# Kernel tuning notes

Measured on AMD Instinct MI355X. Metric: run time of the kernel, lower is better.

Reference implementation:

```python
import jax, jax.numpy as jnp
import numpy as np

N_NODES = 200000
N_EDGES = 400000
IN_CH, HID_CH, OUT_CH = 768, 256, 256
NUM_GRAPHS = 8000


def setup_inputs() -> dict:
    key = jax.random.key(0)
    k = jax.random.split(key, 8)
    x = jax.random.normal(k[0], (N_NODES, IN_CH), dtype=jnp.float32)
    edge_index = jax.random.randint(k[1], (2, N_EDGES), 0, N_NODES, dtype=jnp.int64)
    batch = jnp.sort(jax.random.randint(k[2], (N_NODES,), 0, NUM_GRAPHS, dtype=jnp.int64))
    # GCNConv params (Glorot-ish scale)
    W1 = jax.random.normal(k[3], (IN_CH, HID_CH), dtype=jnp.float32) / np.sqrt(IN_CH)
    b1 = jnp.zeros((HID_CH,), dtype=jnp.float32)
    W2 = jax.random.normal(k[4], (HID_CH, OUT_CH), dtype=jnp.float32) / np.sqrt(HID_CH)
    b2 = jnp.zeros((OUT_CH,), dtype=jnp.float32)
    return {"x": x, "W1": W1, "b1": b1, "W2": W2, "b2": b2,
            "edge_index": edge_index, "batch": batch}


def gcn_conv(x, W, b, src, dst, norm):
    # PyG GCNConv: linear transform, then normalized gather-scatter aggregation
    h = x @ W  # [N, C_out]
    msg = h[src] * norm[:, None]  # gather + scale, [E_sl, C_out]
    out = jax.ops.segment_sum(msg, dst, num_segments=N_NODES)  # scatter-add
    return out + b


def reference(x, W1, b1, W2, b2, edge_index, batch):
    # Add self-loops (PyG GCNConv default add_self_loops=True)
    loops = jnp.arange(N_NODES, dtype=edge_index.dtype)
    src = jnp.concatenate([edge_index[0], loops])
    dst = jnp.concatenate([edge_index[1], loops])
    # Symmetric degree normalization: deg computed on dst (incl. self-loops)
    deg = jax.ops.segment_sum(jnp.ones_like(dst, dtype=x.dtype), dst, num_segments=N_NODES)
    dinv = jnp.where(deg > 0, jax.lax.rsqrt(deg), 0.0)
    norm = dinv[src] * dinv[dst]  # [E_sl]

    h = gcn_conv(x, W1, b1, src, dst, norm)
    h = jax.nn.relu(h)
    h = gcn_conv(h, W2, b2, src, dst, norm)

    # global_mean_pool over batch vector
    sums = jax.ops.segment_sum(h, batch, num_segments=NUM_GRAPHS)
    counts = jax.ops.segment_sum(jnp.ones((N_NODES,), dtype=h.dtype), batch, num_segments=NUM_GRAPHS)
    return sums / jnp.maximum(counts, 1.0)[:, None]
```

## Files before the change

kernel.cpp:

```cpp
#include <hip/hip_runtime.h>


#define N_NODES_C 200000
#define N_EDGES_C 400000
#define IN_CH_C 768
#define HID_C 256
#define NUM_GRAPHS_C 8000

typedef __attribute__((ext_vector_type(8))) short short8;
typedef __attribute__((ext_vector_type(4))) float f32x4;

__device__ __forceinline__ unsigned short f2bf(float f) {
  union { float f; unsigned u; } v; v.f = f;
  unsigned r = v.u + 0x7FFFu + ((v.u >> 16) & 1u);
  return (unsigned short)(r >> 16);
}


__global__ void zero2_kernel(int* __restrict__ a, int* __restrict__ b, int n) {
  int i = blockIdx.x * blockDim.x + threadIdx.x;
  if (i < n) { a[i] = 0; b[i] = 0; }
}

__global__ void hist_kernel(const int* __restrict__ dst, int* __restrict__ deg, int E) {
  int e = blockIdx.x * blockDim.x + threadIdx.x;
  if (e < E) atomicAdd(&deg[dst[e]], 1);
}

__global__ void dinv_kernel(const int* __restrict__ deg, float* __restrict__ dinv, int n) {
  int i = blockIdx.x * blockDim.x + threadIdx.x;
  if (i < n) dinv[i] = rsqrtf((float)(deg[i] + 1));
}

__global__ __launch_bounds__(256) void scan1_kernel(const int* __restrict__ deg,
                                                    int* __restrict__ offs,
                                                    int* __restrict__ bsums, int n) {
  __shared__ int s[256];
  int tid = threadIdx.x;
  int i = blockIdx.x * 256 + tid;
  int v = (i < n) ? deg[i] : 0;
  s[tid] = v;
  __syncthreads();
  for (int d = 1; d < 256; d <<= 1) {
    int t = (tid >= d) ? s[tid - d] : 0;
    __syncthreads();
    s[tid] += t;
    __syncthreads();
  }
  if (i < n) offs[i] = s[tid] - v;
  if (tid == 255) bsums[blockIdx.x] = s[255];
}

__global__ __launch_bounds__(1024) void scan2_kernel(int* __restrict__ bsums, int nb) {
  __shared__ int s[1024];
  int tid = threadIdx.x;
  int v = (tid < nb) ? bsums[tid] : 0;
  s[tid] = v;
  __syncthreads();
  for (int d = 1; d < 1024; d <<= 1) {
    int t = (tid >= d) ? s[tid - d] : 0;
    __syncthreads();
    s[tid] += t;
    __syncthreads();
  }
  if (tid < nb) bsums[tid] = s[tid] - v;
}

__global__ void scan3_kernel(int* __restrict__ offs, const int* __restrict__ bsums, int n) {
  int i = blockIdx.x * 256 + threadIdx.x;
  if (i < n) offs[i] += bsums[blockIdx.x];
  if (i == 0) offs[n] = N_EDGES_C;
}

__global__ void scatter_kernel(const int* __restrict__ esrc_in, const int* __restrict__ edst_in,
                               const int* __restrict__ offs, int* __restrict__ cursor,
                               const float* __restrict__ dinv,
                               int* __restrict__ esrc, float* __restrict__ enorm, int E) {
  int e = blockIdx.x * blockDim.x + threadIdx.x;
  if (e >= E) return;
  int s = esrc_in[e], d = edst_in[e];
  int pos = offs[d] + atomicAdd(&cursor[d], 1);
  esrc[pos] = s;
  enorm[pos] = dinv[s] * dinv[d];
}


__global__ void wprep_kernel(const float* __restrict__ W, unsigned short* __restrict__ WT,
                             int K, int N, int total) {
  int idx = blockIdx.x * blockDim.x + threadIdx.x;
  if (idx >= total) return;
  int n = idx / K, k = idx - n * K;
  WT[idx] = f2bf(W[(size_t)k * N + n]);
}


#define BM 128
#define BN 256
#define BK 32
#define LDT 40

__global__ __launch_bounds__(512) void gemm_bf16_kernel(
    const float* __restrict__ A, const unsigned short* __restrict__ BT,
    float* __restrict__ C, int M, int K) {
  __shared__ unsigned short As[BM * LDT];
  __shared__ unsigned short Bs[BN * LDT];
  const int tid = threadIdx.x;
  const int row0 = blockIdx.x * BM;
  const int lane = tid & 63;
  const int w = tid >> 6;
  const int wm = (w >> 2) * 64;
  const int wn = (w & 3) * 64;
  const int r16 = lane & 15, quad = lane >> 4;

  f32x4 acc[4][4] = {};

  const int arow = tid >> 2;
  const int ak = (tid & 3) * 8;
  const int brow = tid >> 1;
  const int bk = (tid & 1) * 16;

  const bool avalid = (row0 + arow) < M;
  const float* aptr = &A[(size_t)(row0 + arow) * K + ak];
  const unsigned short* bptr = &BT[(size_t)brow * K + bk];

  float av[8];
  uint4 bv0, bv1;
  if (avalid) {
    *(float4*)&av[0] = *(const float4*)&aptr[0];
    *(float4*)&av[4] = *(const float4*)&aptr[4];
  } else {
#pragma unroll
    for (int i = 0; i < 8; ++i) av[i] = 0.f;
  }
  bv0 = *(const uint4*)&bptr[0];
  bv1 = *(const uint4*)&bptr[8];

  for (int k0 = 0; k0 < K; k0 += BK) {
    {
      unsigned short hb[8];
#pragma unroll
      for (int i = 0; i < 8; ++i) hb[i] = f2bf(av[i]);
      *(uint4*)&As[arow * LDT + ak] = *(uint4*)&hb[0];
      *(uint4*)&Bs[brow * LDT + bk] = bv0;
      *(uint4*)&Bs[brow * LDT + bk + 8] = bv1;
    }
    __syncthreads();
    if (k0 + BK < K) {
      if (avalid) {
        *(float4*)&av[0] = *(const float4*)&aptr[k0 + BK + 0];
        *(float4*)&av[4] = *(const float4*)&aptr[k0 + BK + 4];
      }
      bv0 = *(const uint4*)&bptr[k0 + BK + 0];
      bv1 = *(const uint4*)&bptr[k0 + BK + 8];
    }

    short8 af[4], bfr[4];
#pragma unroll
    for (int i = 0; i < 4; ++i)
      af[i] = *(const short8*)&As[(wm + i * 16 + r16) * LDT + quad * 8];
#pragma unroll
    for (int j = 0; j < 4; ++j)
      bfr[j] = *(const short8*)&Bs[(wn + j * 16 + r16) * LDT + quad * 8];
#pragma unroll
    for (int i = 0; i < 4; ++i)
#pragma unroll
      for (int j = 0; j < 4; ++j)
        acc[i][j] = __builtin_amdgcn_mfma_f32_16x16x32_bf16(af[i], bfr[j], acc[i][j], 0, 0, 0);
    __syncthreads();
  }

#pragma unroll
  for (int i = 0; i < 4; ++i) {
#pragma unroll
    for (int r = 0; r < 4; ++r) {
      int gr = row0 + wm + i * 16 + quad * 4 + r;
      if (gr < M) {
#pragma unroll
        for (int j = 0; j < 4; ++j)
          C[(size_t)gr * HID_C + wn + j * 16 + r16] = acc[i][j][r];
      }
    }
  }
}


__global__ __launch_bounds__(256) void aggregate_kernel(
    const float* __restrict__ t, float* __restrict__ out,
    const int* __restrict__ offs, const int* __restrict__ esrc,
    const float* __restrict__ enorm, const float* __restrict__ dinv,
    const float* __restrict__ bias, int do_relu) {
  int wid = (int)(((unsigned)blockIdx.x * blockDim.x + threadIdx.x) >> 6);
  int lane = threadIdx.x & 63;
  if (wid >= N_NODES_C) return;
  int node = wid;
  float di = dinv[node];
  float sn = di * di;
  const float4 tv = *(const float4*)&t[(size_t)node * HID_C + lane * 4];
  float4 acc = make_float4(tv.x * sn, tv.y * sn, tv.z * sn, tv.w * sn);
  int beg = offs[node], end = offs[node + 1];
  for (int p = beg; p < end; ++p) {
    int s = esrc[p];
    float w = enorm[p];
    const float4 v = *(const float4*)&t[(size_t)s * HID_C + lane * 4];
    acc.x += v.x * w; acc.y += v.y * w; acc.z += v.z * w; acc.w += v.w * w;
  }
  const float4 bv = *(const float4*)&bias[lane * 4];
  acc.x += bv.x; acc.y += bv.y; acc.z += bv.z; acc.w += bv.w;
  if (do_relu) {
    acc.x = fmaxf(acc.x, 0.f); acc.y = fmaxf(acc.y, 0.f);
    acc.z = fmaxf(acc.z, 0.f); acc.w = fmaxf(acc.w, 0.f);
  }
  *(float4*)&out[(size_t)node * HID_C + lane * 4] = acc;
}


__device__ __forceinline__ int lower_bound_dev(const int* __restrict__ a, int n, int key) {
  int lo = 0, hi = n;
  while (lo < hi) {
    int mid = (lo + hi) >> 1;
    if (a[mid] < key) lo = mid + 1; else hi = mid;
  }
  return lo;
}

__global__ __launch_bounds__(256) void pool_kernel(const float* __restrict__ h,
                                                   const int* __restrict__ batch,
                                                   float* __restrict__ out) {
  int wid = (int)(((unsigned)blockIdx.x * blockDim.x + threadIdx.x) >> 6);
  int lane = threadIdx.x & 63;
  if (wid >= NUM_GRAPHS_C) return;
  int g = wid;
  int lo = lower_bound_dev(batch, N_NODES_C, g);
  int hi = lower_bound_dev(batch, N_NODES_C, g + 1);
  float4 acc = make_float4(0.f, 0.f, 0.f, 0.f);
  for (int i = lo; i < hi; ++i) {
    const float4 v = *(const float4*)&h[(size_t)i * HID_C + lane * 4];
    acc.x += v.x; acc.y += v.y; acc.z += v.z; acc.w += v.w;
  }
  float inv = 1.0f / fmaxf((float)(hi - lo), 1.0f);
  acc.x *= inv; acc.y *= inv; acc.z *= inv; acc.w *= inv;
  *(float4*)&out[(size_t)g * HID_C + lane * 4] = acc;
}


extern "C" void kernel_launch(void* const* d_in, const int* in_sizes, int n_in,
                              void* d_out, int out_size, void* d_ws, size_t ws_size,
                              hipStream_t stream) {
  (void)in_sizes; (void)n_in; (void)out_size; (void)ws_size;
  const float* x  = (const float*)d_in[0];
  const float* W1 = (const float*)d_in[1];
  const float* b1 = (const float*)d_in[2];
  const float* W2 = (const float*)d_in[3];
  const float* b2 = (const float*)d_in[4];
  const int* edge_index = (const int*)d_in[5];
  const int* batch = (const int*)d_in[6];
  const int* e_src = edge_index;
  const int* e_dst = edge_index + N_EDGES_C;
  float* out = (float*)d_out;

  float* t      = (float*)d_ws;
  float* h      = t + (size_t)N_NODES_C * HID_C;
  float* dinv   = h + (size_t)N_NODES_C * HID_C;
  int*   deg    = (int*)(dinv + N_NODES_C);
  int*   offs   = deg + N_NODES_C;
  int*   cursor = offs + (N_NODES_C + 64);
  int*   esrc   = cursor + N_NODES_C;
  float* enorm  = (float*)(esrc + N_EDGES_C);
  int*   bsums  = (int*)(enorm + N_EDGES_C);
  unsigned short* W1T = (unsigned short*)cursor;
  unsigned short* W2T = W1T + (size_t)IN_CH_C * HID_C;

  const int NB = (N_NODES_C + 255) / 256;
  const int EB = (N_EDGES_C + 255) / 256;

  zero2_kernel<<<NB, 256, 0, stream>>>(deg, cursor, N_NODES_C);
  hist_kernel<<<EB, 256, 0, stream>>>(e_dst, deg, N_EDGES_C);
  scan1_kernel<<<NB, 256, 0, stream>>>(deg, offs, bsums, N_NODES_C);
  scan2_kernel<<<1, 1024, 0, stream>>>(bsums, NB);
  scan3_kernel<<<NB, 256, 0, stream>>>(offs, bsums, N_NODES_C);
  dinv_kernel<<<NB, 256, 0, stream>>>(deg, dinv, N_NODES_C);
  scatter_kernel<<<EB, 256, 0, stream>>>(e_src, e_dst, offs, cursor, dinv, esrc, enorm, N_EDGES_C);

  wprep_kernel<<<(IN_CH_C * HID_C + 255) / 256, 256, 0, stream>>>(W1, W1T, IN_CH_C, HID_C, IN_CH_C * HID_C);
  wprep_kernel<<<(HID_C * HID_C + 255) / 256, 256, 0, stream>>>(W2, W2T, HID_C, HID_C, HID_C * HID_C);

  dim3 g1((N_NODES_C + BM - 1) / BM);
  gemm_bf16_kernel<<<g1, 512, 0, stream>>>(x, W1T, t, N_NODES_C, IN_CH_C);
  aggregate_kernel<<<(N_NODES_C * 64 + 255) / 256, 256, 0, stream>>>(
      t, h, offs, esrc, enorm, dinv, b1, 1);
  gemm_bf16_kernel<<<g1, 512, 0, stream>>>(h, W2T, t, N_NODES_C, HID_C);
  aggregate_kernel<<<(N_NODES_C * 64 + 255) / 256, 256, 0, stream>>>(
      t, h, offs, esrc, enorm, dinv, b2, 0);
  pool_kernel<<<(NUM_GRAPHS_C * 64 + 255) / 256, 256, 0, stream>>>(h, batch, out);
}
```

Before: 1.362 ms.

## Store layer-1 intermediates in bf16 and fuse second aggregation into mean pool

```diff
diff --git a/kernel.cpp b/kernel.cpp
--- a/kernel.cpp
+++ b/kernel.cpp
@@ -14,6 +14,10 @@
   union { float f; unsigned u; } v; v.f = f;
   unsigned r = v.u + 0x7FFFu + ((v.u >> 16) & 1u);
   return (unsigned short)(r >> 16);
+}
+__device__ __forceinline__ float bf2f(unsigned short h) {
+  union { unsigned u; float f; } v; v.u = ((unsigned)h) << 16;
+  return v.f;
 }
 
 
@@ -99,9 +103,10 @@
 #define BK 32
 #define LDT 40
 
-__global__ __launch_bounds__(512) void gemm_bf16_kernel(
-    const float* __restrict__ A, const unsigned short* __restrict__ BT,
-    float* __restrict__ C, int M, int K) {
+template <int ABF16, int CBF16>
+__global__ __launch_bounds__(512) void gemm_kernel(
+    const void* __restrict__ Av, const unsigned short* __restrict__ BT,
+    void* __restrict__ Cv, int M, int K) {
   __shared__ unsigned short As[BM * LDT];
   __shared__ unsigned short Bs[BN * LDT];
   const int tid = threadIdx.x;
@@ -120,35 +125,47 @@
   const int bk = (tid & 1) * 16;
 
   const bool avalid = (row0 + arow) < M;
-  const float* aptr = &A[(size_t)(row0 + arow) * K + ak];
+  const float* aptr32 = &((const float*)Av)[(size_t)(row0 + arow) * K + ak];
+  const unsigned short* aptr16 = &((const unsigned short*)Av)[(size_t)(row0 + arow) * K + ak];
   const unsigned short* bptr = &BT[(size_t)brow * K + bk];
 
   float av[8];
+  uint4 avb = make_uint4(0, 0, 0, 0);
   uint4 bv0, bv1;
-  if (avalid) {
-    *(float4*)&av[0] = *(const float4*)&aptr[0];
-    *(float4*)&av[4] = *(const float4*)&aptr[4];
+  if constexpr (ABF16) {
+    if (avalid) avb = *(const uint4*)&aptr16[0];
   } else {
-#pragma unroll
-    for (int i = 0; i < 8; ++i) av[i] = 0.f;
+    if (avalid) {
+      *(float4*)&av[0] = *(const float4*)&aptr32[0];
+      *(float4*)&av[4] = *(const float4*)&aptr32[4];
+    } else {
+#pragma unroll
+      for (int i = 0; i < 8; ++i) av[i] = 0.f;
+    }
   }
   bv0 = *(const uint4*)&bptr[0];
   bv1 = *(const uint4*)&bptr[8];
 
   for (int k0 = 0; k0 < K; k0 += BK) {
-    {
+    if constexpr (ABF16) {
+      *(uint4*)&As[arow * LDT + ak] = avb;
+    } else {
       unsigned short hb[8];
 #pragma unroll
       for (int i = 0; i < 8; ++i) hb[i] = f2bf(av[i]);
       *(uint4*)&As[arow * LDT + ak] = *(uint4*)&hb[0];
-      *(uint4*)&Bs[brow * LDT + bk] = bv0;
-      *(uint4*)&Bs[brow * LDT + bk + 8] = bv1;
-    }
+    }
+    *(uint4*)&Bs[brow * LDT + bk] = bv0;
+    *(uint4*)&Bs[brow * LDT + bk + 8] = bv1;
     __syncthreads();
     if (k0 + BK < K) {
-      if (avalid) {
-        *(float4*)&av[0] = *(const float4*)&aptr[k0 + BK + 0];
-        *(float4*)&av[4] = *(const float4*)&aptr[k0 + BK + 4];
+      if constexpr (ABF16) {
+        if (avalid) avb = *(const uint4*)&aptr16[k0 + BK];
+      } else {
+        if (avalid) {
+          *(float4*)&av[0] = *(const float4*)&aptr32[k0 + BK + 0];
+          *(float4*)&av[4] = *(const float4*)&aptr32[k0 + BK + 4];
+        }
       }
       bv0 = *(const uint4*)&bptr[k0 + BK + 0];
       bv1 = *(const uint4*)&bptr[k0 + BK + 8];
@@ -175,42 +192,52 @@
     for (int r = 0; r < 4; ++r) {
       int gr = row0 + wm + i * 16 + quad * 4 + r;
       if (gr < M) {
-#pragma unroll
-        for (int j = 0; j < 4; ++j)
-          C[(size_t)gr * HID_C + wn + j * 16 + r16] = acc[i][j][r];
+        if constexpr (CBF16) {
+          unsigned short* C = (unsigned short*)Cv;
+#pragma unroll
+          for (int j = 0; j < 4; ++j)
+            C[(size_t)gr * HID_C + wn + j * 16 + r16] = f2bf(acc[i][j][r]);
+        } else {
+          float* C = (float*)Cv;
+#pragma unroll
+          for (int j = 0; j < 4; ++j)
+            C[(size_t)gr * HID_C + wn + j * 16 + r16] = acc[i][j][r];
+        }
       }
     }
   }
 }
 
 
-__global__ __launch_bounds__(256) void aggregate_kernel(
-    const float* __restrict__ t, float* __restrict__ out,
+__global__ __launch_bounds__(256) void aggregate_bf_kernel(
+    const unsigned short* __restrict__ t, unsigned short* __restrict__ out,
     const int* __restrict__ offs, const int* __restrict__ esrc,
     const float* __restrict__ enorm, const float* __restrict__ dinv,
-    const float* __restrict__ bias, int do_relu) {
+    const float* __restrict__ bias) {
   int wid = (int)(((unsigned)blockIdx.x * blockDim.x + threadIdx.x) >> 6);
   int lane = threadIdx.x & 63;
   if (wid >= N_NODES_C) return;
   int node = wid;
   float di = dinv[node];
   float sn = di * di;
-  const float4 tv = *(const float4*)&t[(size_t)node * HID_C + lane * 4];
-  float4 acc = make_float4(tv.x * sn, tv.y * sn, tv.z * sn, tv.w * sn);
+  ushort4 tv = *(const ushort4*)&t[(size_t)node * HID_C + lane * 4];
+  float4 acc = make_float4(bf2f(tv.x) * sn, bf2f(tv.y) * sn,
+                           bf2f(tv.z) * sn, bf2f(tv.w) * sn);
   int beg = offs[node], end = offs[node + 1];
   for (int p = beg; p < end; ++p) {
     int s = esrc[p];
-    float w = enorm[p];
-    const float4 v = *(const float4*)&t[(size_t)s * HID_C + lane * 4];
-    acc.x += v.x * w; acc.y += v.y * w; acc.z += v.z * w; acc.w += v.w * w;
+    float wgt = enorm[p];
+    ushort4 v = *(const ushort4*)&t[(size_t)s * HID_C + lane * 4];
+    acc.x += bf2f(v.x) * wgt; acc.y += bf2f(v.y) * wgt;
+    acc.z += bf2f(v.z) * wgt; acc.w += bf2f(v.w) * wgt;
   }
   const float4 bv = *(const float4*)&bias[lane * 4];
   acc.x += bv.x; acc.y += bv.y; acc.z += bv.z; acc.w += bv.w;
-  if (do_relu) {
-    acc.x = fmaxf(acc.x, 0.f); acc.y = fmaxf(acc.y, 0.f);
-    acc.z = fmaxf(acc.z, 0.f); acc.w = fmaxf(acc.w, 0.f);
-  }
-  *(float4*)&out[(size_t)node * HID_C + lane * 4] = acc;
+  acc.x = fmaxf(acc.x, 0.f); acc.y = fmaxf(acc.y, 0.f);
+  acc.z = fmaxf(acc.z, 0.f); acc.w = fmaxf(acc.w, 0.f);
+  ushort4 o;
+  o.x = f2bf(acc.x); o.y = f2bf(acc.y); o.z = f2bf(acc.z); o.w = f2bf(acc.w);
+  *(ushort4*)&out[(size_t)node * HID_C + lane * 4] = o;
 }
 
 
@@ -223,23 +250,38 @@
   return lo;
 }
 
-__global__ __launch_bounds__(256) void pool_kernel(const float* __restrict__ h,
-                                                   const int* __restrict__ batch,
-                                                   float* __restrict__ out) {
+__global__ __launch_bounds__(256) void agg_pool_kernel(
+    const float* __restrict__ t, const int* __restrict__ offs,
+    const int* __restrict__ esrc, const float* __restrict__ enorm,
+    const float* __restrict__ dinv, const float* __restrict__ bias,
+    const int* __restrict__ batch, float* __restrict__ out) {
   int wid = (int)(((unsigned)blockIdx.x * blockDim.x + threadIdx.x) >> 6);
   int lane = threadIdx.x & 63;
   if (wid >= NUM_GRAPHS_C) return;
   int g = wid;
   int lo = lower_bound_dev(batch, N_NODES_C, g);
   int hi = lower_bound_dev(batch, N_NODES_C, g + 1);
-  float4 acc = make_float4(0.f, 0.f, 0.f, 0.f);
+  const float4 bv = *(const float4*)&bias[lane * 4];
+  float4 gacc = make_float4(0.f, 0.f, 0.f, 0.f);
   for (int i = lo; i < hi; ++i) {
-    const float4 v = *(const float4*)&h[(size_t)i * HID_C + lane * 4];
-    acc.x += v.x; acc.y += v.y; acc.z += v.z; acc.w += v.w;
+    float di = dinv[i];
+    float sn = di * di;
+    const float4 tv = *(const float4*)&t[(size_t)i * HID_C + lane * 4];
+    float4 acc = make_float4(tv.x * sn, tv.y * sn, tv.z * sn, tv.w * sn);
+    int beg = offs[i], end = offs[i + 1];
+    for (int p = beg; p < end; ++p) {
+      int s = esrc[p];
+      float wgt = enorm[p];
+      const float4 v = *(const float4*)&t[(size_t)s * HID_C + lane * 4];
+      acc.x += v.x * wgt; acc.y += v.y * wgt;
+      acc.z += v.z * wgt; acc.w += v.w * wgt;
+    }
+    gacc.x += acc.x + bv.x; gacc.y += acc.y + bv.y;
+    gacc.z += acc.z + bv.z; gacc.w += acc.w + bv.w;
   }
   float inv = 1.0f / fmaxf((float)(hi - lo), 1.0f);
-  acc.x *= inv; acc.y *= inv; acc.z *= inv; acc.w *= inv;
-  *(float4*)&out[(size_t)g * HID_C + lane * 4] = acc;
+  gacc.x *= inv; gacc.y *= inv; gacc.z *= inv; gacc.w *= inv;
+  *(float4*)&out[(size_t)g * HID_C + lane * 4] = gacc;
 }
 
 
@@ -258,9 +300,11 @@
   const int* e_dst = edge_index + N_EDGES_C;
   float* out = (float*)d_out;
 
-  float* t      = (float*)d_ws;
-  float* h      = t + (size_t)N_NODES_C * HID_C;
-  float* dinv   = h + (size_t)N_NODES_C * HID_C;
+  const size_t NCH = (size_t)N_NODES_C * HID_C;
+  unsigned short* t1 = (unsigned short*)d_ws;
+  unsigned short* h1 = t1 + NCH;
+  float* t2     = (float*)(h1 + NCH);
+  float* dinv   = t2 + NCH;
   int*   deg    = (int*)(dinv + N_NODES_C);
   int*   offs   = deg + N_NODES_C;
   int*   cursor = offs + (N_NODES_C + 64);
@@ -285,11 +329,10 @@
   wprep_kernel<<<(HID_C * HID_C + 255) / 256, 256, 0, stream>>>(W2, W2T, HID_C, HID_C, HID_C * HID_C);
 
   dim3 g1((N_NODES_C + BM - 1) / BM);
-  gemm_bf16_kernel<<<g1, 512, 0, stream>>>(x, W1T, t, N_NODES_C, IN_CH_C);
-  aggregate_kernel<<<(N_NODES_C * 64 + 255) / 256, 256, 0, stream>>>(
-      t, h, offs, esrc, enorm, dinv, b1, 1);
-  gemm_bf16_kernel<<<g1, 512, 0, stream>>>(h, W2T, t, N_NODES_C, HID_C);
-  aggregate_kernel<<<(N_NODES_C * 64 + 255) / 256, 256, 0, stream>>>(
-      t, h, offs, esrc, enorm, dinv, b2, 0);
-  pool_kernel<<<(NUM_GRAPHS_C * 64 + 255) / 256, 256, 0, stream>>>(h, batch, out);
-}
+  gemm_kernel<0, 1><<<g1, 512, 0, stream>>>(x, W1T, t1, N_NODES_C, IN_CH_C);
+  aggregate_bf_kernel<<<(N_NODES_C * 64 + 255) / 256, 256, 0, stream>>>(
+      t1, h1, offs, esrc, enorm, dinv, b1);
+  gemm_kernel<1, 0><<<g1, 512, 0, stream>>>(h1, W2T, t2, N_NODES_C, HID_C);
+  agg_pool_kernel<<<(NUM_GRAPHS_C * 64 + 255) / 256, 256, 0, stream>>>(
+      t2, offs, esrc, enorm, dinv, b2, batch, out);
+}
```

New measurement: 1.198 ms. -12.0%, faster.
